# Optimization experiments

Measured on AMD Instinct MI355X. Metric: run time of the kernel, lower is better.

The kernel has to match this reference:

```python
import jax, jax.numpy as jnp
import numpy as np

B, T, D = 4, 2048, 1024
H = 16
HD = D // H

def setup_inputs() -> dict:
    key = jax.random.key(0)
    ks = jax.random.split(key, 3)
    x = jax.random.normal(ks[0], (B, T, D), dtype=jnp.float32)
    w_qkv = jax.random.normal(ks[1], (D, 3 * D), dtype=jnp.float32) * (1.0 / np.sqrt(D))
    b_qkv = jnp.zeros((3 * D,), dtype=jnp.float32)
    w_proj = jax.random.normal(ks[2], (D, D), dtype=jnp.float32) * (1.0 / np.sqrt(D))
    b_proj = jnp.zeros((D,), dtype=jnp.float32)
    return {"x": x, "w_qkv": w_qkv, "b_qkv": b_qkv, "w_proj": w_proj, "b_proj": b_proj}

def reference(x, w_qkv, b_qkv, w_proj, b_proj):
    b, t, c = x.shape
    qkv = x @ w_qkv + b_qkv                      # [B,T,3D]
    qkv = qkv.reshape(b, t, 3, H, HD).transpose(2, 0, 3, 1, 4)  # [3,B,H,T,HD]
    q, k, v = qkv[0], qkv[1], qkv[2]
    scale = jnp.sqrt(jnp.asarray(HD, dtype=x.dtype))
    attn = jnp.einsum('bhqd,bhkd->bhqk', q, k) / scale  # [B,H,T,T]
    causal = jnp.tril(jnp.ones((t, t), dtype=bool))
    attn = jnp.where(causal[None, None], attn, -jnp.inf)
    attn = jax.nn.softmax(attn, axis=-1)
    out = jnp.einsum('bhqk,bhkd->bhqd', attn, v)        # [B,H,T,HD]
    out = out.transpose(0, 2, 1, 3).reshape(b, t, c)
    return out @ w_proj + b_proj
```

## Files before the change

### kernel.cpp

```cpp
#include <hip/hip_runtime.h>

typedef float f32x4 __attribute__((ext_vector_type(4)));
typedef __bf16 bf16x8 __attribute__((ext_vector_type(8)));

static __device__ __forceinline__ unsigned short f2bf(float f) {
    unsigned int u = __builtin_bit_cast(unsigned int, f);
    u += 0x7fffu + ((u >> 16) & 1u);
    return (unsigned short)(u >> 16);
}
static __device__ __forceinline__ unsigned short bfc(float f) {
    return __builtin_bit_cast(unsigned short, (__bf16)f);
}

#define QSC 0.18033688011112042f

typedef const __attribute__((address_space(1))) unsigned int gu32;
typedef __attribute__((address_space(3))) unsigned int lu32;
static __device__ __forceinline__ void gload_lds16(const unsigned short* g, unsigned short* l) {
    __builtin_amdgcn_global_load_lds((gu32*)g, (lu32*)l, 16, 0, 0);
}

__global__ __launch_bounds__(256)
void cvt_bf16(const float* __restrict__ in, unsigned short* __restrict__ out) {
    int i = blockIdx.x * 256 + threadIdx.x;
    const float4* p = (const float4*)in + (size_t)i * 2;
    float4 a = p[0], b = p[1];
    union { unsigned short s[8]; uint4 v; } u;
    u.s[0] = f2bf(a.x); u.s[1] = f2bf(a.y); u.s[2] = f2bf(a.z); u.s[3] = f2bf(a.w);
    u.s[4] = f2bf(b.x); u.s[5] = f2bf(b.y); u.s[6] = f2bf(b.z); u.s[7] = f2bf(b.w);
    ((uint4*)out)[i] = u.v;
}

__global__ __launch_bounds__(256)
void transpose_w(const float* __restrict__ w, unsigned short* __restrict__ wT,
                 int K, int N) {
    __shared__ unsigned short Lt[64][65];
    const int k0 = blockIdx.x * 64, n0 = blockIdx.y * 64;
    const int t = threadIdx.x;
    const int r = t >> 4, c4 = (t & 15) * 4;
    #pragma unroll
    for (int i = 0; i < 4; i++) {
        int rr = r + i * 16;
        float4 v = *(const float4*)(w + (k0 + rr) * N + n0 + c4);
        Lt[rr][c4 + 0] = f2bf(v.x); Lt[rr][c4 + 1] = f2bf(v.y);
        Lt[rr][c4 + 2] = f2bf(v.z); Lt[rr][c4 + 3] = f2bf(v.w);
    }
    __syncthreads();
    const int rn = t >> 3, ks = (t & 7) * 8;
    #pragma unroll
    for (int i = 0; i < 2; i++) {
        int rr = rn + i * 32;
        unsigned short tmp[8];
        #pragma unroll
        for (int j = 0; j < 8; j++) tmp[j] = Lt[ks + j][rr];
        *(uint4*)(wT + (n0 + rr) * K + k0 + ks) = *(const uint4*)tmp;
    }
}

__global__ __launch_bounds__(256)
void qkv_gemm2(const unsigned short* __restrict__ A,
               const unsigned short* __restrict__ Bt,
               const float* __restrict__ bias,
               unsigned short* __restrict__ q_ws,
               unsigned short* __restrict__ k_ws,
               unsigned short* __restrict__ vT_ws)
{
    const int K = 1024;
    __shared__ unsigned short Al[2][128 * 32];
    __shared__ unsigned short Bl[2][128 * 32];
    const int tid = threadIdx.x;
    const int lane = tid & 63, w = tid >> 6;
    const int l15 = lane & 15, lhi = lane >> 4;
    const int m0 = blockIdx.x * 128, n0 = blockIdx.y * 128;
    const int wm = (w >> 1) * 64, wn = (w & 1) * 64;

    const int srow = w * 32 + (lane >> 2);
    const int sg = ((lane & 3) ^ ((lane >> 3) & 3)) * 8;
    const unsigned short* ga = A + (size_t)(m0 + srow) * K + sg;
    const unsigned short* gb = Bt + (size_t)(n0 + srow) * K + sg;
    const int lofs = w * 32 * 32;

    const int rc = (lhi ^ ((l15 >> 1) & 3)) * 8;

    f32x4 acc[4][4] = {};

    gload_lds16(ga, &Al[0][lofs]);
    gload_lds16(ga + 16 * K, &Al[0][lofs + 512]);
    gload_lds16(gb, &Bl[0][lofs]);
    gload_lds16(gb + 16 * K, &Bl[0][lofs + 512]);
    __syncthreads();

    int cur = 0;
    for (int k0 = 0; k0 < K; k0 += 32) {
        const int nxt = cur ^ 1;
        if (k0 + 32 < K) {
            gload_lds16(ga + k0 + 32,          &Al[nxt][lofs]);
            gload_lds16(ga + k0 + 32 + 16 * K, &Al[nxt][lofs + 512]);
            gload_lds16(gb + k0 + 32,          &Bl[nxt][lofs]);
            gload_lds16(gb + k0 + 32 + 16 * K, &Bl[nxt][lofs + 512]);
        }
        bf16x8 af[4], bfr[4];
        #pragma unroll
        for (int m = 0; m < 4; m++)
            af[m] = *(const bf16x8*)(&Al[cur][(wm + m * 16 + l15) * 32 + rc]);
        #pragma unroll
        for (int n = 0; n < 4; n++)
            bfr[n] = *(const bf16x8*)(&Bl[cur][(wn + n * 16 + l15) * 32 + rc]);
        __builtin_amdgcn_s_setprio(1);
        #pragma unroll
        for (int m = 0; m < 4; m++)
            #pragma unroll
            for (int n = 0; n < 4; n++)
                acc[m][n] = __builtin_amdgcn_mfma_f32_16x16x32_bf16(af[m], bfr[n], acc[m][n], 0, 0, 0);
        __builtin_amdgcn_s_setprio(0);
        __syncthreads();
        cur = nxt;
    }

    #pragma unroll
    for (int n = 0; n < 4; n++) {
        int col = n0 + wn + n * 16 + l15;
        float bv = bias[col];
        int which = col >> 10;
        int d = col & 1023;
        int h = d >> 6, hd = d & 63;
        #pragma unroll
        for (int m = 0; m < 4; m++) {
            #pragma unroll
            for (int j = 0; j < 4; j++) {
                int row = m0 + wm + m * 16 + lhi * 4 + j;
                int b = row >> 11, t = row & 2047;
                float val = acc[m][n][j] + bv;
                int bh = b * 16 + h;
                if (which == 0)      q_ws[(bh * 2048 + t) * 64 + hd] = f2bf(val * QSC);
                else if (which == 1) k_ws[(bh * 2048 + t) * 64 + hd] = f2bf(val);
                else                 vT_ws[(bh * 64 + hd) * 2048 + t] = f2bf(val);
            }
        }
    }
}

#define LKK 72

__global__ __launch_bounds__(512, 4)
void attn_fwd(const unsigned short* __restrict__ q_ws,
              const unsigned short* __restrict__ k_ws,
              const unsigned short* __restrict__ vT_ws,
              unsigned short* __restrict__ attn_ws)
{
    __shared__ unsigned short Kb[2][64 * LKK];
    __shared__ unsigned short Vb[2][64 * LKK];
    __shared__ unsigned short Pl[8][16 * 64];

    const int bh = blockIdx.x;
    const int p  = blockIdx.y;
    const int b = bh >> 4, h = bh & 15;
    const int tid = threadIdx.x;
    const int lane = tid & 63, wid = tid >> 6;
    const int l15 = lane & 15, lhi = lane >> 4;
    const int tbase = bh * 2048;
    const float NINF = -__builtin_inff();

    const int r0 = tid >> 3;
    const int c0 = (tid & 7) * 8;
    const unsigned short* kg = k_ws + (size_t)(tbase + r0) * 64 + c0;
    const unsigned short* vg = vT_ws + ((size_t)bh * 64 + r0) * 2048 + c0;

    unsigned short* Pw = &Pl[wid][0];
    const int xr = l15 & 7;

    #pragma unroll 1
    for (int seg = 0; seg < 2; ++seg) {
        const int qb = seg ? p : 15 - p;
        const int q0 = qb * 128;
        const int qrow = q0 + wid * 16;
        const int nkv = 2 * (qb + 1);

        bf16x8 qf[2];
        #pragma unroll
        for (int ks = 0; ks < 2; ks++)
            qf[ks] = *(const bf16x8*)(q_ws + (size_t)(tbase + qrow + l15) * 64 + ks * 32 + lhi * 8);

        f32x4 o[4] = {};
        float mreg = NINF, lst = 0.f;

        {
            uint4 ka = *(const uint4*)(kg);
            uint4 va = *(const uint4*)(vg);
            *(uint4*)(&Kb[0][r0 * LKK + c0]) = ka;
            *(uint4*)(&Vb[0][r0 * LKK + c0]) = va;
        }
        __syncthreads();

        int cur = 0;
        for (int kb = 0; kb < nkv; ++kb) {
            const int k0 = kb * 64;
            const int knx = (kb + 1 < nkv ? kb + 1 : kb) * 64;
            uint4 ka = *(const uint4*)(kg + (size_t)knx * 64);
            uint4 va = *(const uint4*)(vg + knx);

            if (k0 <= qrow + 15) {
                f32x4 s[4] = {};
                __builtin_amdgcn_s_setprio(1);
                #pragma unroll
                for (int ks = 0; ks < 2; ks++) {
                    bf16x8 kf[4];
                    #pragma unroll
                    for (int n = 0; n < 4; n++)
                        kf[n] = *(const bf16x8*)(&Kb[cur][(n * 16 + l15) * LKK + ks * 32 + lhi * 8]);
                    #pragma unroll
                    for (int n = 0; n < 4; n++)
                        s[n] = __builtin_amdgcn_mfma_f32_16x16x32_bf16(kf[n], qf[ks], s[n], 0, 0, 0);
                }
                __builtin_amdgcn_s_setprio(0);
                if (k0 + 63 > qrow) {
                    int qg = qrow + l15;
                    #pragma unroll
                    for (int n = 0; n < 4; n++) {
                        int kgl = k0 + n * 16 + lhi * 4;
                        #pragma unroll
                        for (int j = 0; j < 4; j++)
                            s[n][j] = (kgl + j <= qg) ? s[n][j] : NINF;
                    }
                }
                float mx = NINF;
                #pragma unroll
                for (int n = 0; n < 4; n++)
                    #pragma unroll
                    for (int j = 0; j < 4; j++)
                        mx = fmaxf(mx, s[n][j]);
                mx = fmaxf(mx, __shfl_xor(mx, 16));
                mx = fmaxf(mx, __shfl_xor(mx, 32));

                if (__all(mx <= mreg + 8.f)) {
                    float rs = 0.f;
                    #pragma unroll
                    for (int n = 0; n < 4; n++)
                        #pragma unroll
                        for (int j = 0; j < 4; j++) {
                            float pv = exp2f(s[n][j] - mreg);
                            s[n][j] = pv;
                            rs += pv;
                        }
                    rs += __shfl_xor(rs, 16);
                    rs += __shfl_xor(rs, 32);
                    lst += rs;
                } else {
                    float mnew = fmaxf(mreg, mx);
                    float al = exp2f(mreg - mnew);
                    mreg = mnew;
                    float rs = 0.f;
                    #pragma unroll
                    for (int n = 0; n < 4; n++)
                        #pragma unroll
                        for (int j = 0; j < 4; j++) {
                            float pv = exp2f(s[n][j] - mnew);
                            s[n][j] = pv;
                            rs += pv;
                        }
                    rs += __shfl_xor(rs, 16);
                    rs += __shfl_xor(rs, 32);
                    lst = lst * al + rs;
                    #pragma unroll
                    for (int j = 0; j < 4; j++) {
                        float a = __shfl(al, lhi * 4 + j);
                        #pragma unroll
                        for (int nd = 0; nd < 4; nd++)
                            o[nd][j] *= a;
                    }
                }
                #pragma unroll
                for (int n = 0; n < 4; n++) {
                    ushort4 pk;
                    pk.x = bfc(s[n][0]); pk.y = bfc(s[n][1]);
                    pk.z = bfc(s[n][2]); pk.w = bfc(s[n][3]);
                    int chunk = (2 * n + (lhi >> 1)) ^ xr;
                    *(ushort4*)(&Pw[l15 * 64 + chunk * 8 + (lhi & 1) * 4]) = pk;
                }
                __builtin_amdgcn_s_setprio(1);
                #pragma unroll
                for (int ks = 0; ks < 2; ks++) {
                    int chunk = (4 * ks + lhi) ^ xr;
                    bf16x8 pf = *(const bf16x8*)(&Pw[l15 * 64 + chunk * 8]);
                    bf16x8 vf[4];
                    #pragma unroll
                    for (int nd = 0; nd < 4; nd++)
                        vf[nd] = *(const bf16x8*)(&Vb[cur][(nd * 16 + l15) * LKK + ks * 32 + lhi * 8]);
                    #pragma unroll
                    for (int nd = 0; nd < 4; nd++)
                        o[nd] = __builtin_amdgcn_mfma_f32_16x16x32_bf16(pf, vf[nd], o[nd], 0, 0, 0);
                }
                __builtin_amdgcn_s_setprio(0);
            }
            *(uint4*)(&Kb[cur ^ 1][r0 * LKK + c0]) = ka;
            *(uint4*)(&Vb[cur ^ 1][r0 * LKK + c0]) = va;
            __syncthreads();
            cur ^= 1;
        }
        #pragma unroll
        for (int j = 0; j < 4; j++) {
            float lv = __shfl(lst, lhi * 4 + j);
            float inv = 1.0f / lv;
            int t = qrow + lhi * 4 + j;
            #pragma unroll
            for (int nd = 0; nd < 4; nd++) {
                int d = nd * 16 + l15;
                attn_ws[((size_t)(b * 2048 + t) * 16 + h) * 64 + d] = f2bf(o[nd][j] * inv);
            }
        }
    }
}

__global__ __launch_bounds__(256)
void proj_gemm2(const unsigned short* __restrict__ A,
                const unsigned short* __restrict__ Bt,
                const float* __restrict__ bias, float* __restrict__ out)
{
    const int K = 1024, N = 1024;
    __shared__ unsigned short Al[2][128 * 32];
    __shared__ unsigned short Bl[2][128 * 32];
    const int tid = threadIdx.x;
    const int lane = tid & 63, w = tid >> 6;
    const int l15 = lane & 15, lhi = lane >> 4;
    const int m0 = blockIdx.x * 128, n0 = blockIdx.y * 128;
    const int wm = (w >> 1) * 64, wn = (w & 1) * 64;

    const int srow = w * 32 + (lane >> 2);
    const int sg = ((lane & 3) ^ ((lane >> 3) & 3)) * 8;
    const unsigned short* ga = A + (size_t)(m0 + srow) * K + sg;
    const unsigned short* gb = Bt + (size_t)(n0 + srow) * K + sg;
    const int lofs = w * 32 * 32;

    const int rc = (lhi ^ ((l15 >> 1) & 3)) * 8;

    f32x4 acc[4][4] = {};

    gload_lds16(ga, &Al[0][lofs]);
    gload_lds16(ga + 16 * K, &Al[0][lofs + 512]);
    gload_lds16(gb, &Bl[0][lofs]);
    gload_lds16(gb + 16 * K, &Bl[0][lofs + 512]);
    __syncthreads();

    int cur = 0;
    for (int k0 = 0; k0 < K; k0 += 32) {
        const int nxt = cur ^ 1;
        if (k0 + 32 < K) {
            gload_lds16(ga + k0 + 32,          &Al[nxt][lofs]);
            gload_lds16(ga + k0 + 32 + 16 * K, &Al[nxt][lofs + 512]);
            gload_lds16(gb + k0 + 32,          &Bl[nxt][lofs]);
            gload_lds16(gb + k0 + 32 + 16 * K, &Bl[nxt][lofs + 512]);
        }
        bf16x8 af[4], bfr[4];
        #pragma unroll
        for (int m = 0; m < 4; m++)
            af[m] = *(const bf16x8*)(&Al[cur][(wm + m * 16 + l15) * 32 + rc]);
        #pragma unroll
        for (int n = 0; n < 4; n++)
            bfr[n] = *(const bf16x8*)(&Bl[cur][(wn + n * 16 + l15) * 32 + rc]);
        __builtin_amdgcn_s_setprio(1);
        #pragma unroll
        for (int m = 0; m < 4; m++)
            #pragma unroll
            for (int n = 0; n < 4; n++)
                acc[m][n] = __builtin_amdgcn_mfma_f32_16x16x32_bf16(af[m], bfr[n], acc[m][n], 0, 0, 0);
        __builtin_amdgcn_s_setprio(0);
        __syncthreads();
        cur = nxt;
    }

    #pragma unroll
    for (int n = 0; n < 4; n++) {
        int col = n0 + wn + n * 16 + l15;
        float bv = bias[col];
        #pragma unroll
        for (int m = 0; m < 4; m++)
            #pragma unroll
            for (int j = 0; j < 4; j++) {
                int row = m0 + wm + m * 16 + lhi * 4 + j;
                out[row * N + col] = acc[m][n][j] + bv;
            }
    }
}

extern "C" void kernel_launch(void* const* d_in, const int* in_sizes, int n_in,
                              void* d_out, int out_size, void* d_ws, size_t ws_size,
                              hipStream_t stream)
{
    const float* x      = (const float*)d_in[0];
    const float* w_qkv  = (const float*)d_in[1];
    const float* b_qkv  = (const float*)d_in[2];
    const float* w_proj = (const float*)d_in[3];
    const float* b_proj = (const float*)d_in[4];
    float* out = (float*)d_out;

    const size_t SEG = (size_t)8 * 1024 * 1024;
    unsigned short* q_ws    = (unsigned short*)d_ws;
    unsigned short* k_ws    = q_ws + SEG;
    unsigned short* vT_ws   = k_ws + SEG;
    unsigned short* attn_ws = vT_ws + SEG;

    unsigned short* x_bf   = (unsigned short*)d_out;
    unsigned short* wqkvT  = x_bf + SEG;
    unsigned short* wprojT = q_ws;

    cvt_bf16<<<4096, 256, 0, stream>>>(x, x_bf);
    transpose_w<<<dim3(16, 48), 256, 0, stream>>>(w_qkv, wqkvT, 1024, 3072);
    qkv_gemm2<<<dim3(64, 24), 256, 0, stream>>>(x_bf, wqkvT, b_qkv, q_ws, k_ws, vT_ws);
    attn_fwd<<<dim3(64, 8), 512, 0, stream>>>(q_ws, k_ws, vT_ws, attn_ws);
    transpose_w<<<dim3(16, 16), 256, 0, stream>>>(w_proj, wprojT, 1024, 1024);
    proj_gemm2<<<dim3(64, 8), 256, 0, stream>>>(attn_ws, wprojT, b_proj, out);
}
```

Before: 199.1 us.

## Triple-buffer LDS in QKV and projection GEMMs with one barrier per step

Both GEMM kernels move from double to triple LDS buffering. Global-to-LDS loads are now issued two k-steps ahead, and a manual vmcnt wait plus a single s_barrier replaces the end-of-iteration __syncthreads. This is meant to hide more global load latency behind MFMA work and remove one sync per step. In exchange it raises LDS use from 32KB to 48KB per block, which may lower occupancy, and its correctness depends on the hand-written vmcnt counts and on the barrier placement preventing write-after-read hazards.

```diff
diff --git a/kernel.cpp b/kernel.cpp
--- a/kernel.cpp
+++ b/kernel.cpp
@@ -66,8 +66,8 @@
                unsigned short* __restrict__ vT_ws)
 {
     const int K = 1024;
-    __shared__ unsigned short Al[2][128 * 32];
-    __shared__ unsigned short Bl[2][128 * 32];
+    __shared__ unsigned short Al[3][128 * 32];
+    __shared__ unsigned short Bl[3][128 * 32];
     const int tid = threadIdx.x;
     const int lane = tid & 63, w = tid >> 6;
     const int l15 = lane & 15, lhi = lane >> 4;
@@ -84,28 +84,31 @@
 
     f32x4 acc[4][4] = {};
 
-    gload_lds16(ga, &Al[0][lofs]);
-    gload_lds16(ga + 16 * K, &Al[0][lofs + 512]);
-    gload_lds16(gb, &Bl[0][lofs]);
-    gload_lds16(gb + 16 * K, &Bl[0][lofs + 512]);
-    __syncthreads();
-
-    int cur = 0;
+    #define STG(kk, bb) do { \
+        gload_lds16(ga + (kk),          &Al[bb][lofs]); \
+        gload_lds16(ga + (kk) + 16 * K, &Al[bb][lofs + 512]); \
+        gload_lds16(gb + (kk),          &Bl[bb][lofs]); \
+        gload_lds16(gb + (kk) + 16 * K, &Bl[bb][lofs + 512]); \
+    } while (0)
+
+    STG(0, 0);
+    STG(32, 1);
+
+    int bi = 0;
     for (int k0 = 0; k0 < K; k0 += 32) {
-        const int nxt = cur ^ 1;
-        if (k0 + 32 < K) {
-            gload_lds16(ga + k0 + 32,          &Al[nxt][lofs]);
-            gload_lds16(ga + k0 + 32 + 16 * K, &Al[nxt][lofs + 512]);
-            gload_lds16(gb + k0 + 32,          &Bl[nxt][lofs]);
-            gload_lds16(gb + k0 + 32 + 16 * K, &Bl[nxt][lofs + 512]);
-        }
+        if (k0 + 32 < K) asm volatile("s_waitcnt vmcnt(4)" ::: "memory");
+        else             asm volatile("s_waitcnt vmcnt(0)" ::: "memory");
+        asm volatile("s_barrier" ::: "memory");
+        int bs = bi + 2; if (bs >= 3) bs -= 3;
+        if (k0 + 64 < K) STG(k0 + 64, bs);
+
         bf16x8 af[4], bfr[4];
         #pragma unroll
         for (int m = 0; m < 4; m++)
-            af[m] = *(const bf16x8*)(&Al[cur][(wm + m * 16 + l15) * 32 + rc]);
+            af[m] = *(const bf16x8*)(&Al[bi][(wm + m * 16 + l15) * 32 + rc]);
         #pragma unroll
         for (int n = 0; n < 4; n++)
-            bfr[n] = *(const bf16x8*)(&Bl[cur][(wn + n * 16 + l15) * 32 + rc]);
+            bfr[n] = *(const bf16x8*)(&Bl[bi][(wn + n * 16 + l15) * 32 + rc]);
         __builtin_amdgcn_s_setprio(1);
         #pragma unroll
         for (int m = 0; m < 4; m++)
@@ -113,9 +116,9 @@
             for (int n = 0; n < 4; n++)
                 acc[m][n] = __builtin_amdgcn_mfma_f32_16x16x32_bf16(af[m], bfr[n], acc[m][n], 0, 0, 0);
         __builtin_amdgcn_s_setprio(0);
-        __syncthreads();
-        cur = nxt;
-    }
+        bi = (bi + 1 == 3) ? 0 : bi + 1;
+    }
+    #undef STG
 
     #pragma unroll
     for (int n = 0; n < 4; n++) {
@@ -317,8 +320,8 @@
                 const float* __restrict__ bias, float* __restrict__ out)
 {
     const int K = 1024, N = 1024;
-    __shared__ unsigned short Al[2][128 * 32];
-    __shared__ unsigned short Bl[2][128 * 32];
+    __shared__ unsigned short Al[3][128 * 32];
+    __shared__ unsigned short Bl[3][128 * 32];
     const int tid = threadIdx.x;
     const int lane = tid & 63, w = tid >> 6;
     const int l15 = lane & 15, lhi = lane >> 4;
@@ -335,28 +338,31 @@
 
     f32x4 acc[4][4] = {};
 
-    gload_lds16(ga, &Al[0][lofs]);
-    gload_lds16(ga + 16 * K, &Al[0][lofs + 512]);
-    gload_lds16(gb, &Bl[0][lofs]);
-    gload_lds16(gb + 16 * K, &Bl[0][lofs + 512]);
-    __syncthreads();
-
-    int cur = 0;
+    #define STG(kk, bb) do { \
+        gload_lds16(ga + (kk),          &Al[bb][lofs]); \
+        gload_lds16(ga + (kk) + 16 * K, &Al[bb][lofs + 512]); \
+        gload_lds16(gb + (kk),          &Bl[bb][lofs]); \
+        gload_lds16(gb + (kk) + 16 * K, &Bl[bb][lofs + 512]); \
+    } while (0)
+
+    STG(0, 0);
+    STG(32, 1);
+
+    int bi = 0;
     for (int k0 = 0; k0 < K; k0 += 32) {
-        const int nxt = cur ^ 1;
-        if (k0 + 32 < K) {
-            gload_lds16(ga + k0 + 32,          &Al[nxt][lofs]);
-            gload_lds16(ga + k0 + 32 + 16 * K, &Al[nxt][lofs + 512]);
-            gload_lds16(gb + k0 + 32,          &Bl[nxt][lofs]);
-            gload_lds16(gb + k0 + 32 + 16 * K, &Bl[nxt][lofs + 512]);
-        }
+        if (k0 + 32 < K) asm volatile("s_waitcnt vmcnt(4)" ::: "memory");
+        else             asm volatile("s_waitcnt vmcnt(0)" ::: "memory");
+        asm volatile("s_barrier" ::: "memory");
+        int bs = bi + 2; if (bs >= 3) bs -= 3;
+        if (k0 + 64 < K) STG(k0 + 64, bs);
+
         bf16x8 af[4], bfr[4];
         #pragma unroll
         for (int m = 0; m < 4; m++)
-            af[m] = *(const bf16x8*)(&Al[cur][(wm + m * 16 + l15) * 32 + rc]);
+            af[m] = *(const bf16x8*)(&Al[bi][(wm + m * 16 + l15) * 32 + rc]);
         #pragma unroll
         for (int n = 0; n < 4; n++)
-            bfr[n] = *(const bf16x8*)(&Bl[cur][(wn + n * 16 + l15) * 32 + rc]);
+            bfr[n] = *(const bf16x8*)(&Bl[bi][(wn + n * 16 + l15) * 32 + rc]);
         __builtin_amdgcn_s_setprio(1);
         #pragma unroll
         for (int m = 0; m < 4; m++)
@@ -364,9 +370,9 @@
             for (int n = 0; n < 4; n++)
                 acc[m][n] = __builtin_amdgcn_mfma_f32_16x16x32_bf16(af[m], bfr[n], acc[m][n], 0, 0, 0);
         __builtin_amdgcn_s_setprio(0);
-        __syncthreads();
-        cur = nxt;
-    }
+        bi = (bi + 1 == 3) ? 0 : bi + 1;
+    }
+    #undef STG
 
     #pragma unroll
     for (int n = 0; n < 4; n++) {
```

Result: no change. 201.0 us (+1.0%).
